# Optimization experiments

Hardware: AMD Instinct MI355X
Metric: run time of the kernel (lower is better)

## Reference

```python
import jax, jax.numpy as jnp
import numpy as np

D_MODEL = 1024
NUM_HEADS = 16
D_K = D_MODEL // NUM_HEADS
SCALE = D_K ** -0.5
NEG = -1e9


def _split_heads(t):
    B, L, D = t.shape
    return t.reshape(B, L, NUM_HEADS, D_K).transpose(0, 2, 1, 3)  # (B,H,L,dk)


def _tropical_scores(Q, K):
    # max over d_k of Q[...,i,d] + K[...,j,d] without materializing (B,H,L,L,dk)
    Qd = jnp.moveaxis(Q, -1, 0)  # (dk,B,H,L)
    Kd = jnp.moveaxis(K, -1, 0)
    B, H, L, _ = Q.shape
    init = jnp.full((B, H, L, L), -jnp.inf, Q.dtype)
    def step(carry, qk):
        q, k = qk  # (B,H,L) each
        return jnp.maximum(carry, q[..., :, None] + k[..., None, :]), None
    out, _ = jax.lax.scan(step, init, (Qd, Kd))
    return out


def setup_inputs() -> dict:
    key = jax.random.key(0)
    ks = jax.random.split(key, 10)
    B, L = 2, 1024
    x = jax.random.normal(ks[0], (B, L, D_MODEL), dtype=jnp.float32)
    # causal mask (B,1,L,L)
    mask = jnp.broadcast_to(jnp.tril(jnp.ones((L, L), dtype=bool)), (B, 1, L, L))
    s = 0.02
    Wq = jax.random.normal(ks[1], (D_MODEL, D_MODEL), jnp.float32) * s
    Wk = jax.random.normal(ks[2], (D_MODEL, D_MODEL), jnp.float32) * s
    Wv = jax.random.normal(ks[3], (D_MODEL, D_MODEL), jnp.float32) * s
    Wo = jax.random.normal(ks[4], (D_MODEL, D_MODEL), jnp.float32) * s
    bq = jnp.zeros((D_MODEL,), jnp.float32)
    bk = jnp.zeros((D_MODEL,), jnp.float32)
    bv = jnp.zeros((D_MODEL,), jnp.float32)
    bo = jnp.zeros((D_MODEL,), jnp.float32)
    # score_gate: weight zero-init, bias = -2.0 (as in torch module)
    Wg = jnp.zeros((NUM_HEADS, D_MODEL), jnp.float32)
    bg = jnp.full((NUM_HEADS,), -2.0, jnp.float32)
    # log temperatures, init_temp=1.0 -> log(1)=0
    log_temps = jnp.zeros((NUM_HEADS,), jnp.float32)
    return {"x": x, "mask": mask, "Wq": Wq, "bq": bq, "Wk": Wk, "bk": bk,
            "Wv": Wv, "bv": bv, "Wo": Wo, "bo": bo, "Wg": Wg, "bg": bg,
            "log_temps": log_temps}


def reference(x, mask, Wq, bq, Wk, bk, Wv, bv, Wo, bo, Wg, bg, log_temps):
    B, L, D = x.shape
    Q = _split_heads(x @ Wq.T + bq)
    K = _split_heads(x @ Wk.T + bk)
    V = _split_heads(x @ Wv.T + bv)
    class_scores = jnp.einsum('bhqd,bhkd->bhqk', Q, K) * SCALE
    trop_scores = _tropical_scores(Q, K) * SCALE
    # per-query, per-head gate g in (0,1): (B,L,H) -> (B,H,L,1)
    g = jax.nn.sigmoid(x @ Wg.T + bg).transpose(0, 2, 1)[..., None]
    scores = g * trop_scores + (1.0 - g) * class_scores
    scores = jnp.where(mask, scores, NEG)
    tau = jnp.clip(jnp.exp(log_temps), 0.02, 10.0).reshape(1, NUM_HEADS, 1, 1)
    attn = jax.nn.softmax(scores / tau, axis=-1)
    out = jnp.einsum('bhqk,bhkd->bhqd', attn, V)
    out = out.transpose(0, 2, 1, 3).reshape(B, L, D)
    return out @ Wo.T + bo, attn
```

## Files before the change

kernel.cpp:

```cpp
#include <hip/hip_runtime.h>


typedef _Float16 f16;
typedef __attribute__((ext_vector_type(2))) _Float16 h2;
typedef __attribute__((ext_vector_type(8))) _Float16 f16x8;
typedef __attribute__((ext_vector_type(4))) float f32x4;

__device__ inline f32x4 mfma_f16(f16x8 a, f16x8 b, f32x4 c) {
    return __builtin_amdgcn_mfma_f32_16x16x32_f16(a, b, c, 0, 0, 0);
}

__device__ inline void async_copy16(const f16* g, f16* l) {
    __builtin_amdgcn_global_load_lds((const __attribute__((address_space(1))) void*)g,
                                     (__attribute__((address_space(3))) void*)l, 16, 0, 0);
}

__global__ __launch_bounds__(256) void cvt_all(const float* __restrict__ x,
                                               const float* __restrict__ Wq,
                                               const float* __restrict__ Wk,
                                               const float* __restrict__ Wv,
                                               const float* __restrict__ Wo,
                                               f16* __restrict__ x16,
                                               f16* __restrict__ w16,
                                               f16* __restrict__ wo16) {
    int i = blockIdx.x * 256 + threadIdx.x;
    const float* s;
    f16* d;
    int off;
    if (i < 524288)       { s = x;  d = x16;             off = i; }
    else if (i < 786432)  { s = Wq; d = w16;             off = i - 524288; }
    else if (i < 1048576) { s = Wk; d = w16 + (1 << 20); off = i - 786432; }
    else if (i < 1310720) { s = Wv; d = w16 + (2 << 20); off = i - 1048576; }
    else                  { s = Wo; d = wo16;            off = i - 1310720; }
    float4 v = *(const float4*)(s + (size_t)off * 4);
    f16 o[4] = {(f16)v.x, (f16)v.y, (f16)v.z, (f16)v.w};
    *(uint2*)(d + (size_t)off * 4) = *(uint2*)o;
}

template <bool OUT16, bool VTR>
__global__ __launch_bounds__(256) void gemm128(const f16* __restrict__ A,
                                               const f16* __restrict__ B,
                                               void* __restrict__ Cv,
                                               const float* __restrict__ b0,
                                               const float* __restrict__ b1,
                                               const float* __restrict__ b2,
                                               f16* __restrict__ vt,
                                               int K, int lda, int ldb, int ldc) {
    __shared__ f16 At[128 * 32];
    __shared__ f16 Bt[64 * 32];
    const int t = threadIdx.x;
    const int m0 = blockIdx.y * 128, n0 = blockIdx.x * 64;
    const int wave = t >> 6, lane = t & 63;
    const int l16 = lane & 15, quad = lane >> 4;
    const int wm = (wave >> 1) * 64, wn = (wave & 1) * 32;
    const int sr = t >> 2, sc = (t & 3) * 8;
    f32x4 acc[4][2] = {};
    for (int k0 = 0; k0 < K; k0 += 32) {
        __syncthreads();
#pragma unroll
        for (int i = 0; i < 2; ++i)
            async_copy16(A + (size_t)(m0 + sr + i * 64) * lda + k0 + sc, &At[t * 8 + i * 2048]);
        async_copy16(B + (size_t)(n0 + sr) * ldb + k0 + sc, &Bt[t * 8]);
        __syncthreads();
        f16x8 af[4], bfr[2];
#pragma unroll
        for (int i = 0; i < 4; ++i)
            af[i] = *(const f16x8*)&At[(wm + i * 16 + l16) * 32 + quad * 8];
#pragma unroll
        for (int i = 0; i < 2; ++i)
            bfr[i] = *(const f16x8*)&Bt[(wn + i * 16 + l16) * 32 + quad * 8];
#pragma unroll
        for (int mi = 0; mi < 4; ++mi)
#pragma unroll
            for (int ni = 0; ni < 2; ++ni)
                acc[mi][ni] = mfma_f16(af[mi], bfr[ni], acc[mi][ni]);
    }
#pragma unroll
    for (int mi = 0; mi < 4; ++mi) {
#pragma unroll
        for (int ni = 0; ni < 2; ++ni) {
            int gcol = n0 + wn + ni * 16 + l16;
            const float* bp = (gcol < 1024) ? b0 : (gcol < 2048 ? b1 : b2);
            float bias = bp[gcol & 1023];
            if (VTR && n0 >= 2048) {
                int hd = gcol - 2048;
                int h = hd >> 6, d = hd & 63;
                int k0r = m0 + wm + mi * 16 + quad * 4;
                int b = k0r >> 10;
                f16 o4[4];
#pragma unroll
                for (int rg = 0; rg < 4; ++rg) o4[rg] = (f16)(acc[mi][ni][rg] + bias);
                *(uint2*)&vt[((size_t)((b * 16 + h) * 64 + d)) * 1024 + (k0r & 1023)] =
                    *(uint2*)o4;
            } else {
#pragma unroll
                for (int rg = 0; rg < 4; ++rg) {
                    int grow = m0 + wm + mi * 16 + quad * 4 + rg;
                    float v = acc[mi][ni][rg] + bias;
                    if (OUT16)
                        ((f16*)Cv)[(size_t)grow * ldc + gcol] = (f16)v;
                    else
                        ((float*)Cv)[(size_t)grow * ldc + gcol] = v;
                }
            }
        }
    }
}

__global__ __launch_bounds__(256) void scores_fused(const f16* __restrict__ qkv16,
                                                    const f16* __restrict__ vt16,
                                                    const float* __restrict__ x,
                                                    const float* __restrict__ Wg,
                                                    const float* __restrict__ bgv,
                                                    const float* __restrict__ log_temps,
                                                    float* __restrict__ attn,
                                                    f16* __restrict__ oh) {
    __shared__ f16 Qs[16][80];
    __shared__ f16 Ssm[16][1032];
    __shared__ float gsm[16];
    const int t = threadIdx.x;
    const int qt = 63 - (blockIdx.x >> 5);
    const int bh = blockIdx.x & 31;
    const int b = bh & 1, h = bh >> 1;
    const int q0 = qt << 4;
    const int lane = t & 63, w = t >> 6;
    const int l16 = lane & 15, quad = lane >> 4;
    const int qmax = q0 + 15;

    {
        int rr = t >> 4, cc = (t & 15) * 4;
        *(uint2*)&Qs[rr][cc] =
            *(const uint2*)(qkv16 + (size_t)(b * 1024 + q0 + rr) * 3072 + h * 64 + cc);
    }
    {
        int row = t >> 4, ch = t & 15;
        const float* xp = x + (size_t)(b * 1024 + q0 + row) * 1024 + ch * 64;
        const float* wp = Wg + (size_t)h * 1024 + ch * 64;
        float acc = 0.f;
#pragma unroll
        for (int j = 0; j < 16; ++j) {
            float4 xv = *(const float4*)(xp + j * 4);
            float4 wv = *(const float4*)(wp + j * 4);
            acc = fmaf(xv.x, wv.x, acc);
            acc = fmaf(xv.y, wv.y, acc);
            acc = fmaf(xv.z, wv.z, acc);
            acc = fmaf(xv.w, wv.w, acc);
        }
#pragma unroll
        for (int o = 8; o > 0; o >>= 1) acc += __shfl_xor(acc, o);
        if (ch == 0) gsm[row] = 1.0f / (1.0f + __expf(-(acc + bgv[h])));
    }
    float tau = __expf(log_temps[h]);
    tau = fminf(fmaxf(tau, 0.02f), 10.0f);
    const float invtau = 1.0f / tau;
    __syncthreads();

    {
        f16x8 qf0 = *(const f16x8*)&Qs[l16][quad * 8];
        f16x8 qf1 = *(const f16x8*)&Qs[l16][32 + quad * 8];
        const f16* Kb = qkv16 + (size_t)(b * 1024 + l16) * 3072 + 1024 + h * 64 + quad * 8;
        for (int kb = w * 16; kb <= qmax; kb += 64) {
            f16x8 kf0 = *(const f16x8*)(Kb + (size_t)kb * 3072);
            f16x8 kf1 = *(const f16x8*)(Kb + (size_t)kb * 3072 + 32);
            f32x4 acc = {};
            acc = mfma_f16(kf0, qf0, acc);
            acc = mfma_f16(kf1, qf1, acc);
            f16 o4[4];
#pragma unroll
            for (int rg = 0; rg < 4; ++rg) o4[rg] = (f16)acc[rg];
            *(uint2*)&Ssm[l16][kb + quad * 4] = *(uint2*)o4;
        }
    }
    __syncthreads();

    {
        const int q = t & 15, kg = t >> 4;
        h2 qr[32];
#pragma unroll
        for (int i = 0; i < 8; ++i) *(f16x8*)&qr[i * 4] = *(const f16x8*)&Qs[q][i * 8];
        const float g = gsm[q];
        const f16* Kp = qkv16 + (size_t)(b * 1024) * 3072 + 1024 + h * 64;
        h2 krA[32], krB[32];
        const int nit = qt + 1;

#define KLOAD(KR, row)                                                        \
    {                                                                         \
        const f16* kp_ = Kp + (size_t)(row) * 3072;                           \
        _Pragma("unroll") for (int i_ = 0; i_ < 8; ++i_)                      \
            *(f16x8*)&KR[i_ * 4] = ((const f16x8*)kp_)[i_];                   \
    }
#define TROP(KR, kk)                                                          \
    {                                                                         \
        float dot = (float)Ssm[q][kk];                                        \
        h2 ta = qr[0] + KR[0], tb = qr[1] + KR[1];                            \
        _Pragma("unroll") for (int i_ = 2; i_ < 32; i_ += 2) {                \
            ta = __builtin_elementwise_max(ta, qr[i_] + KR[i_]);              \
            tb = __builtin_elementwise_max(tb, qr[i_ + 1] + KR[i_ + 1]);      \
        }                                                                     \
        h2 tc = __builtin_elementwise_max(ta, tb);                            \
        float tm = fmaxf((float)tc[0], (float)tc[1]);                         \
        Ssm[q][kk] = (f16)((g * tm + (1.0f - g) * dot) * 0.125f);             \
    }

        KLOAD(krA, kg);
        for (int it = 0; it < nit; it += 2) {
            int k = it * 16 + kg;
            if (it + 1 < nit) KLOAD(krB, k + 16);
            TROP(krA, k);
            if (it + 1 < nit) {
                if (it + 2 < nit) KLOAD(krA, k + 32);
                TROP(krB, k + 16);
            }
        }
#undef KLOAD
#undef TROP
    }
    __syncthreads();

#pragma unroll
    for (int j = 0; j < 4; ++j) {
        int q = w * 4 + j;
        int qg = q0 + q;
        float m = -1e30f;
        for (int k = lane; k <= qg; k += 64) m = fmaxf(m, (float)Ssm[q][k]);
#pragma unroll
        for (int o = 32; o > 0; o >>= 1) m = fmaxf(m, __shfl_xor(m, o));
        float e[16];
        float ssum = 0.f;
#pragma unroll
        for (int i = 0; i < 16; ++i) {
            int k = lane + i * 64;
            if (k <= qg) {
                float v = __expf(((float)Ssm[q][k] - m) * invtau);
                e[i] = v;
                ssum += v;
            } else
                e[i] = 0.f;
        }
#pragma unroll
        for (int o = 32; o > 0; o >>= 1) ssum += __shfl_xor(ssum, o);
        float inv = 1.0f / ssum;
        float* orow = attn + ((size_t)((b * 16 + h) * 1024 + qg) << 10);
#pragma unroll
        for (int i = 0; i < 16; ++i) {
            int k = lane + i * 64;
            float val = e[i] * inv;
            orow[k] = val;
            Ssm[q][k] = (f16)val;
        }
    }
    __syncthreads();

    {
        const int dw = w * 16;
        f32x4 acc = {};
        const int nkt = (q0 + 47) >> 5;
        const f16* Vb = vt16 + ((size_t)((b * 16 + h) * 64 + dw + l16)) * 1024 + quad * 8;
#pragma unroll 4
        for (int kt = 0; kt < nkt; ++kt) {
            const int kb = kt << 5;
            f16x8 a = *(const f16x8*)&Ssm[l16][kb + quad * 8];
            f16x8 bf = *(const f16x8*)(Vb + kb);
            acc = mfma_f16(a, bf, acc);
        }
#pragma unroll
        for (int rg = 0; rg < 4; ++rg)
            oh[(size_t)(b * 1024 + q0 + quad * 4 + rg) * 1024 + h * 64 + dw + l16] =
                (f16)acc[rg];
    }
}

extern "C" void kernel_launch(void* const* d_in, const int* in_sizes, int n_in,
                              void* d_out, int out_size, void* d_ws, size_t ws_size,
                              hipStream_t stream) {
    const float* x  = (const float*)d_in[0];
    const float* Wq = (const float*)d_in[2];
    const float* bq = (const float*)d_in[3];
    const float* Wk = (const float*)d_in[4];
    const float* bk = (const float*)d_in[5];
    const float* Wv = (const float*)d_in[6];
    const float* bv = (const float*)d_in[7];
    const float* Wo = (const float*)d_in[8];
    const float* bo = (const float*)d_in[9];
    const float* Wg = (const float*)d_in[10];
    const float* bg = (const float*)d_in[11];
    const float* lt = (const float*)d_in[12];
    float* out = (float*)d_out;
    float* attn = out + (size_t)2 * 1024 * 1024;

    char* ws = (char*)d_ws;
    const size_t MB = (size_t)1 << 20;
    f16*   x16   = (f16*)ws;
    f16*   w16   = (f16*)(ws + 4 * MB);
    f16*   wo16  = (f16*)(ws + 10 * MB);
    f16*   qkv16 = (f16*)(ws + 12 * MB);
    f16*   vt16  = (f16*)(ws + 24 * MB);
    f16*   oh16  = (f16*)(ws + 29 * MB);

    cvt_all<<<6144, 256, 0, stream>>>(x, Wq, Wk, Wv, Wo, x16, w16, wo16);
    gemm128<true, true><<<dim3(48, 16), 256, 0, stream>>>(x16, w16, qkv16, bq, bk, bv,
                                                          vt16, 1024, 1024, 1024, 3072);
    scores_fused<<<2048, 256, 0, stream>>>(qkv16, vt16, x, Wg, bg, lt, attn, oh16);
    gemm128<false, false><<<dim3(16, 16), 256, 0, stream>>>(oh16, wo16, out, bo, bo, bo,
                                                            nullptr, 1024, 1024, 1024, 1024);
}
```

Before: 339.7 us.

## Restructure tropical score loop per key and widen QKV GEMM tile

The tropical max-plus loop is remapped so each thread owns 4 consecutive keys, held in registers, and loops over all 16 queries read from LDS. Previously each thread owned one query and streamed key rows from global memory. This cuts repeated global K loads, but the 128-half key register array raises register pressure, and threads beyond the causal limit now sit idle. The QKV projection gets a dedicated 128x128-tile GEMM (a 24x16 grid) for more reuse per block, and scores_fused now requests 2 blocks per SIMD via launch bounds.

```diff
diff --git a/kernel.cpp b/kernel.cpp
--- a/kernel.cpp
+++ b/kernel.cpp
@@ -37,14 +37,75 @@
     *(uint2*)(d + (size_t)off * 4) = *(uint2*)o;
 }
 
-template <bool OUT16, bool VTR>
+__global__ __launch_bounds__(256) void gemm_qkv(const f16* __restrict__ A,
+                                                const f16* __restrict__ B,
+                                                f16* __restrict__ C,
+                                                const float* __restrict__ b0,
+                                                const float* __restrict__ b1,
+                                                const float* __restrict__ b2,
+                                                f16* __restrict__ vt) {
+    __shared__ f16 At[128 * 32];
+    __shared__ f16 Bt[128 * 32];
+    const int t = threadIdx.x;
+    const int m0 = blockIdx.y * 128, n0 = blockIdx.x * 128;
+    const int wave = t >> 6, lane = t & 63;
+    const int l16 = lane & 15, quad = lane >> 4;
+    const int wm = (wave >> 1) * 64, wn = (wave & 1) * 64;
+    const int sr = t >> 2, sc = (t & 3) * 8;
+    f32x4 acc[4][4] = {};
+    for (int k0 = 0; k0 < 1024; k0 += 32) {
+        __syncthreads();
+#pragma unroll
+        for (int i = 0; i < 2; ++i) {
+            async_copy16(A + (size_t)(m0 + sr + i * 64) * 1024 + k0 + sc, &At[t * 8 + i * 2048]);
+            async_copy16(B + (size_t)(n0 + sr + i * 64) * 1024 + k0 + sc, &Bt[t * 8 + i * 2048]);
+        }
+        __syncthreads();
+        f16x8 af[4], bf[4];
+#pragma unroll
+        for (int i = 0; i < 4; ++i) {
+            af[i] = *(const f16x8*)&At[(wm + i * 16 + l16) * 32 + quad * 8];
+            bf[i] = *(const f16x8*)&Bt[(wn + i * 16 + l16) * 32 + quad * 8];
+        }
+#pragma unroll
+        for (int mi = 0; mi < 4; ++mi)
+#pragma unroll
+            for (int ni = 0; ni < 4; ++ni)
+                acc[mi][ni] = mfma_f16(af[mi], bf[ni], acc[mi][ni]);
+    }
+#pragma unroll
+    for (int mi = 0; mi < 4; ++mi) {
+#pragma unroll
+        for (int ni = 0; ni < 4; ++ni) {
+            int gcol = n0 + wn + ni * 16 + l16;
+            const float* bp = (gcol < 1024) ? b0 : (gcol < 2048 ? b1 : b2);
+            float bias = bp[gcol & 1023];
+            if (n0 >= 2048) {
+                int hd = gcol - 2048;
+                int hh = hd >> 6, dd = hd & 63;
+                int k0r = m0 + wm + mi * 16 + quad * 4;
+                int bb = k0r >> 10;
+                f16 o4[4];
+#pragma unroll
+                for (int rg = 0; rg < 4; ++rg) o4[rg] = (f16)(acc[mi][ni][rg] + bias);
+                *(uint2*)&vt[((size_t)((bb * 16 + hh) * 64 + dd)) * 1024 + (k0r & 1023)] =
+                    *(uint2*)o4;
+            } else {
+#pragma unroll
+                for (int rg = 0; rg < 4; ++rg) {
+                    int grow = m0 + wm + mi * 16 + quad * 4 + rg;
+                    C[(size_t)grow * 3072 + gcol] = (f16)(acc[mi][ni][rg] + bias);
+                }
+            }
+        }
+    }
+}
+
+template <bool OUT16>
 __global__ __launch_bounds__(256) void gemm128(const f16* __restrict__ A,
                                                const f16* __restrict__ B,
                                                void* __restrict__ Cv,
                                                const float* __restrict__ b0,
-                                               const float* __restrict__ b1,
-                                               const float* __restrict__ b2,
-                                               f16* __restrict__ vt,
                                                int K, int lda, int ldb, int ldc) {
     __shared__ f16 At[128 * 32];
     __shared__ f16 Bt[64 * 32];
@@ -80,41 +141,28 @@
 #pragma unroll
         for (int ni = 0; ni < 2; ++ni) {
             int gcol = n0 + wn + ni * 16 + l16;
-            const float* bp = (gcol < 1024) ? b0 : (gcol < 2048 ? b1 : b2);
-            float bias = bp[gcol & 1023];
-            if (VTR && n0 >= 2048) {
-                int hd = gcol - 2048;
-                int h = hd >> 6, d = hd & 63;
-                int k0r = m0 + wm + mi * 16 + quad * 4;
-                int b = k0r >> 10;
-                f16 o4[4];
-#pragma unroll
-                for (int rg = 0; rg < 4; ++rg) o4[rg] = (f16)(acc[mi][ni][rg] + bias);
-                *(uint2*)&vt[((size_t)((b * 16 + h) * 64 + d)) * 1024 + (k0r & 1023)] =
-                    *(uint2*)o4;
-            } else {
-#pragma unroll
-                for (int rg = 0; rg < 4; ++rg) {
-                    int grow = m0 + wm + mi * 16 + quad * 4 + rg;
-                    float v = acc[mi][ni][rg] + bias;
-                    if (OUT16)
-                        ((f16*)Cv)[(size_t)grow * ldc + gcol] = (f16)v;
-                    else
-                        ((float*)Cv)[(size_t)grow * ldc + gcol] = v;
-                }
+            float bias = b0[gcol];
+#pragma unroll
+            for (int rg = 0; rg < 4; ++rg) {
+                int grow = m0 + wm + mi * 16 + quad * 4 + rg;
+                float v = acc[mi][ni][rg] + bias;
+                if (OUT16)
+                    ((f16*)Cv)[(size_t)grow * ldc + gcol] = (f16)v;
+                else
+                    ((float*)Cv)[(size_t)grow * ldc + gcol] = v;
             }
         }
     }
 }
 
-__global__ __launch_bounds__(256) void scores_fused(const f16* __restrict__ qkv16,
-                                                    const f16* __restrict__ vt16,
-                                                    const float* __restrict__ x,
-                                                    const float* __restrict__ Wg,
-                                                    const float* __restrict__ bgv,
-                                                    const float* __restrict__ log_temps,
-                                                    float* __restrict__ attn,
-                                                    f16* __restrict__ oh) {
+__global__ __launch_bounds__(256, 2) void scores_fused(const f16* __restrict__ qkv16,
+                                                       const f16* __restrict__ vt16,
+                                                       const float* __restrict__ x,
+                                                       const float* __restrict__ Wg,
+                                                       const float* __restrict__ bgv,
+                                                       const float* __restrict__ log_temps,
+                                                       float* __restrict__ attn,
+                                                       f16* __restrict__ oh) {
     __shared__ f16 Qs[16][80];
     __shared__ f16 Ssm[16][1032];
     __shared__ float gsm[16];
@@ -174,46 +222,40 @@
     __syncthreads();
 
     {
-        const int q = t & 15, kg = t >> 4;
-        h2 qr[32];
-#pragma unroll
-        for (int i = 0; i < 8; ++i) *(f16x8*)&qr[i * 4] = *(const f16x8*)&Qs[q][i * 8];
-        const float g = gsm[q];
-        const f16* Kp = qkv16 + (size_t)(b * 1024) * 3072 + 1024 + h * 64;
-        h2 krA[32], krB[32];
-        const int nit = qt + 1;
-
-#define KLOAD(KR, row)                                                        \
-    {                                                                         \
-        const f16* kp_ = Kp + (size_t)(row) * 3072;                           \
-        _Pragma("unroll") for (int i_ = 0; i_ < 8; ++i_)                      \
-            *(f16x8*)&KR[i_ * 4] = ((const f16x8*)kp_)[i_];                   \
-    }
-#define TROP(KR, kk)                                                          \
-    {                                                                         \
-        float dot = (float)Ssm[q][kk];                                        \
-        h2 ta = qr[0] + KR[0], tb = qr[1] + KR[1];                            \
-        _Pragma("unroll") for (int i_ = 2; i_ < 32; i_ += 2) {                \
-            ta = __builtin_elementwise_max(ta, qr[i_] + KR[i_]);              \
-            tb = __builtin_elementwise_max(tb, qr[i_ + 1] + KR[i_ + 1]);      \
-        }                                                                     \
-        h2 tc = __builtin_elementwise_max(ta, tb);                            \
-        float tm = fmaxf((float)tc[0], (float)tc[1]);                         \
-        Ssm[q][kk] = (f16)((g * tm + (1.0f - g) * dot) * 0.125f);             \
-    }
-
-        KLOAD(krA, kg);
-        for (int it = 0; it < nit; it += 2) {
-            int k = it * 16 + kg;
-            if (it + 1 < nit) KLOAD(krB, k + 16);
-            TROP(krA, k);
-            if (it + 1 < nit) {
-                if (it + 2 < nit) KLOAD(krA, k + 32);
-                TROP(krB, k + 16);
+        const int k0 = t * 4;
+        if (k0 <= qmax) {
+            h2 kr[4][32];
+            const f16* Kp = qkv16 + (size_t)(b * 1024 + k0) * 3072 + 1024 + h * 64;
+#pragma unroll
+            for (int j = 0; j < 4; ++j)
+#pragma unroll
+                for (int i = 0; i < 8; ++i)
+                    *(f16x8*)&kr[j][i * 4] = *(const f16x8*)(Kp + (size_t)j * 3072 + i * 8);
+#pragma unroll 2
+            for (int q = 0; q < 16; ++q) {
+                h2 qr[32];
+#pragma unroll
+                for (int i = 0; i < 8; ++i)
+                    *(f16x8*)&qr[i * 4] = *(const f16x8*)&Qs[q][i * 8];
+                const float g = gsm[q];
+                f16 d4[4];
+                *(uint2*)d4 = *(const uint2*)&Ssm[q][k0];
+                f16 o4[4];
+#pragma unroll
+                for (int j = 0; j < 4; ++j) {
+                    h2 ta = qr[0] + kr[j][0], tb = qr[1] + kr[j][1];
+#pragma unroll
+                    for (int i = 2; i < 32; i += 2) {
+                        ta = __builtin_elementwise_max(ta, qr[i] + kr[j][i]);
+                        tb = __builtin_elementwise_max(tb, qr[i + 1] + kr[j][i + 1]);
+                    }
+                    h2 tc = __builtin_elementwise_max(ta, tb);
+                    float tm = fmaxf((float)tc[0], (float)tc[1]);
+                    o4[j] = (f16)((g * tm + (1.0f - g) * (float)d4[j]) * 0.125f);
+                }
+                *(uint2*)&Ssm[q][k0] = *(uint2*)o4;
             }
         }
-#undef KLOAD
-#undef TROP
     }
     __syncthreads();
 
@@ -298,9 +340,7 @@
     f16*   oh16  = (f16*)(ws + 29 * MB);
 
     cvt_all<<<6144, 256, 0, stream>>>(x, Wq, Wk, Wv, Wo, x16, w16, wo16);
-    gemm128<true, true><<<dim3(48, 16), 256, 0, stream>>>(x16, w16, qkv16, bq, bk, bv,
-                                                          vt16, 1024, 1024, 1024, 3072);
+    gemm_qkv<<<dim3(24, 16), 256, 0, stream>>>(x16, w16, qkv16, bq, bk, bv, vt16);
     scores_fused<<<2048, 256, 0, stream>>>(qkv16, vt16, x, Wg, bg, lt, attn, oh16);
-    gemm128<false, false><<<dim3(16, 16), 256, 0, stream>>>(oh16, wo16, out, bo, bo, bo,
-                                                            nullptr, 1024, 1024, 1024, 1024);
-}
+    gemm128<false><<<dim3(16, 16), 256, 0, stream>>>(oh16, wo16, out, bo, 1024, 1024, 1024, 1024);
+}
```

New measurement: 347.0 us. 1.02x slower.

## Remap tropical score loop so each thread owns keys and iterates over queries

Applied to the files above, without the earlier changes.

The tropical max-plus score pass used to give each thread one query and stream 16-strided key rows from global memory. It now gives each thread up to two key rows, held in registers across a pass, and loops over the 16 queries read from shared memory. This cuts redundant global K loads, since each K row is loaded once per block instead of once per query lane group. The trade-offs are heavier register pressure, broadcast LDS reads of Q, and idle threads in the masked causal tail.

```diff
diff --git a/kernel.cpp b/kernel.cpp
--- a/kernel.cpp
+++ b/kernel.cpp
@@ -174,46 +174,55 @@
     __syncthreads();
 
     {
-        const int q = t & 15, kg = t >> 4;
-        h2 qr[32];
-#pragma unroll
-        for (int i = 0; i < 8; ++i) *(f16x8*)&qr[i * 4] = *(const f16x8*)&Qs[q][i * 8];
-        const float g = gsm[q];
-        const f16* Kp = qkv16 + (size_t)(b * 1024) * 3072 + 1024 + h * 64;
-        h2 krA[32], krB[32];
-        const int nit = qt + 1;
-
-#define KLOAD(KR, row)                                                        \
-    {                                                                         \
-        const f16* kp_ = Kp + (size_t)(row) * 3072;                           \
-        _Pragma("unroll") for (int i_ = 0; i_ < 8; ++i_)                      \
-            *(f16x8*)&KR[i_ * 4] = ((const f16x8*)kp_)[i_];                   \
-    }
-#define TROP(KR, kk)                                                          \
-    {                                                                         \
-        float dot = (float)Ssm[q][kk];                                        \
-        h2 ta = qr[0] + KR[0], tb = qr[1] + KR[1];                            \
-        _Pragma("unroll") for (int i_ = 2; i_ < 32; i_ += 2) {                \
-            ta = __builtin_elementwise_max(ta, qr[i_] + KR[i_]);              \
-            tb = __builtin_elementwise_max(tb, qr[i_ + 1] + KR[i_ + 1]);      \
-        }                                                                     \
-        h2 tc = __builtin_elementwise_max(ta, tb);                            \
-        float tm = fmaxf((float)tc[0], (float)tc[1]);                         \
-        Ssm[q][kk] = (f16)((g * tm + (1.0f - g) * dot) * 0.125f);             \
-    }
-
-        KLOAD(krA, kg);
-        for (int it = 0; it < nit; it += 2) {
-            int k = it * 16 + kg;
-            if (it + 1 < nit) KLOAD(krB, k + 16);
-            TROP(krA, k);
-            if (it + 1 < nit) {
-                if (it + 2 < nit) KLOAD(krA, k + 32);
-                TROP(krB, k + 16);
+        const int npass = (qmax >> 9) + 1;
+        for (int p = 0; p < npass; ++p) {
+            const int k1 = (p << 9) + t;
+            const int k2 = k1 + 256;
+            const bool a1 = (k1 <= qmax), a2 = (k2 <= qmax);
+            if (a1) {
+                const f16* Kp1 = qkv16 + (size_t)(b * 1024 + k1) * 3072 + 1024 + h * 64;
+                h2 kr1[32], kr2[32];
+#pragma unroll
+                for (int i = 0; i < 8; ++i) *(f16x8*)&kr1[i * 4] = ((const f16x8*)Kp1)[i];
+                if (a2) {
+                    const f16* Kp2 = qkv16 + (size_t)(b * 1024 + k2) * 3072 + 1024 + h * 64;
+#pragma unroll
+                    for (int i = 0; i < 8; ++i) *(f16x8*)&kr2[i * 4] = ((const f16x8*)Kp2)[i];
+                }
+#pragma unroll 2
+                for (int q = 0; q < 16; ++q) {
+                    h2 qr[32];
+#pragma unroll
+                    for (int i = 0; i < 8; ++i)
+                        *(f16x8*)&qr[i * 4] = *(const f16x8*)&Qs[q][i * 8];
+                    const float g = gsm[q];
+                    {
+                        float dot = (float)Ssm[q][k1];
+                        h2 ta = qr[0] + kr1[0], tb = qr[1] + kr1[1];
+#pragma unroll
+                        for (int i = 2; i < 32; i += 2) {
+                            ta = __builtin_elementwise_max(ta, qr[i] + kr1[i]);
+                            tb = __builtin_elementwise_max(tb, qr[i + 1] + kr1[i + 1]);
+                        }
+                        h2 tc = __builtin_elementwise_max(ta, tb);
+                        float tm = fmaxf((float)tc[0], (float)tc[1]);
+                        Ssm[q][k1] = (f16)((g * tm + (1.0f - g) * dot) * 0.125f);
+                    }
+                    if (a2) {
+                        float dot = (float)Ssm[q][k2];
+                        h2 ta = qr[0] + kr2[0], tb = qr[1] + kr2[1];
+#pragma unroll
+                        for (int i = 2; i < 32; i += 2) {
+                            ta = __builtin_elementwise_max(ta, qr[i] + kr2[i]);
+                            tb = __builtin_elementwise_max(tb, qr[i + 1] + kr2[i + 1]);
+                        }
+                        h2 tc = __builtin_elementwise_max(ta, tb);
+                        float tm = fmaxf((float)tc[0], (float)tc[1]);
+                        Ssm[q][k2] = (f16)((g * tm + (1.0f - g) * dot) * 0.125f);
+                    }
+                }
             }
         }
-#undef KLOAD
-#undef TROP
     }
     __syncthreads();
 
```

Measured after the change: 320.6 us. -5.6%, faster.
